# Kernel tuning notes

Hardware: AMD Instinct MI355X
Metric: run time of the kernel (lower is better)

Reference implementation:

```python
import jax, jax.numpy as jnp
import numpy as np

B, S, D, H = 4, 1024, 1024, 16
DK = D // H


def setup_inputs() -> dict:
    key = jax.random.key(0)
    ks = jax.random.split(key, 13)
    s = 1.0 / np.sqrt(D)
    return {
        "query": jax.random.normal(ks[0], (B, S, D), jnp.float32),
        "key": jax.random.normal(ks[1], (B, S, D), jnp.float32),
        "value": jax.random.normal(ks[2], (B, S, D), jnp.float32),
        "mask": jax.random.randint(ks[3], (B, H, S, S), 0, 2).astype(bool),
        "Wq": jax.random.normal(ks[4], (D, D), jnp.float32) * s,
        "bq": jnp.zeros((D,), jnp.float32),
        "Wk": jax.random.normal(ks[5], (D, D), jnp.float32) * s,
        "bk": jnp.zeros((D,), jnp.float32),
        "Wv": jax.random.normal(ks[6], (D, D), jnp.float32) * s,
        "bv": jnp.zeros((D,), jnp.float32),
        "Wo": jax.random.normal(ks[7], (D, D), jnp.float32) * s,
        "bo": jnp.zeros((D,), jnp.float32),
    }


def reference(query, key, value, mask, Wq, bq, Wk, bk, Wv, bv, Wo, bo):
    b = query.shape[0]
    # QKV projections, split heads: [B,S,D] -> [B,H,S,DK]
    q = (query @ Wq + bq).reshape(b, -1, H, DK).transpose(0, 2, 1, 3)
    k = (key @ Wk + bk).reshape(b, -1, H, DK).transpose(0, 2, 1, 3)
    v = (value @ Wv + bv).reshape(b, -1, H, DK).transpose(0, 2, 1, 3)
    # scaled dot-product attention with explicit [B,H,Sq,Sk] scores
    scores = jnp.einsum("bhqd,bhkd->bhqk", q, k) / jnp.sqrt(jnp.float32(DK))
    scores = jnp.where(mask, -jnp.inf, scores)
    attn_weights = jax.nn.softmax(scores, axis=-1)
    attn_out = jnp.einsum("bhqk,bhkd->bhqd", attn_weights, v)
    # merge heads and project out; dropout is identity in eval mode
    attn_out = attn_out.transpose(0, 2, 1, 3).reshape(b, -1, D)
    out = attn_out @ Wo + bo
    return out, attn_weights
```

## Files before the change

### kernel.cpp

```cpp
#include <hip/hip_runtime.h>

typedef __attribute__((ext_vector_type(8))) __bf16   bf16x8;
typedef __attribute__((ext_vector_type(4))) __bf16   bf16x4;
typedef __attribute__((ext_vector_type(8))) _Float16 halfx8;
typedef __attribute__((ext_vector_type(4))) float    floatx4;
typedef __attribute__((ext_vector_type(4))) int      intx4;

#define S_  1024
#define D_  1024
#define H_  16
#define DK_ 64
#define B_  4
#define M_  4096

__device__ __forceinline__ void gload_lds16(const void* g, void* l) {
  __builtin_amdgcn_global_load_lds(
      (const __attribute__((address_space(1))) unsigned int*)g,
      (__attribute__((address_space(3))) unsigned int*)l, 16, 0, 0);
}

__global__ __launch_bounds__(256) void prep(
    const float* __restrict__ q, const float* __restrict__ k,
    const float* __restrict__ v, __bf16* __restrict__ X,
    const float* __restrict__ W0, const float* __restrict__ W1,
    const float* __restrict__ W2, const float* __restrict__ W3,
    __bf16* __restrict__ WT, const unsigned char* __restrict__ m,
    int* __restrict__ flag)
{
  __shared__ __align__(16) unsigned char shb[9216];
  const int bid = blockIdx.x;
  const int t = threadIdx.x;
  if (bid < 6144) {
    const int z = bid >> 11;
    const int bx = bid & 2047;
    const float* src = (z == 0) ? q : (z == 1) ? k : v;
    __bf16* dst = X + (size_t)z * 4194304;
    const size_t idx = ((size_t)bx * 256 + t) * 8;
    floatx4 a = *(const floatx4*)(src + idx);
    floatx4 b = *(const floatx4*)(src + idx + 4);
    bf16x8 o;
#pragma unroll
    for (int j = 0; j < 4; ++j) { o[j] = (__bf16)a[j]; o[4 + j] = (__bf16)b[j]; }
    *(bf16x8*)(dst + idx) = o;
  } else if (bid < 7168) {
    const int g = bid - 6144;
    const int z = g >> 8, yy = (g >> 4) & 15, xx = g & 15;
    const float* W = (z == 0) ? W0 : (z == 1) ? W1 : (z == 2) ? W2 : W3;
    __bf16* O = WT + (size_t)z * (D_ * (size_t)D_);
    __bf16* T = (__bf16*)shb;
    const int r0 = yy * 64, c0 = xx * 64;
#pragma unroll
    for (int it = 0; it < 4; ++it) {
      int idx = t * 4 + it * 1024;
      int r = idx >> 6, c = idx & 63;
      floatx4 a = *(const floatx4*)(W + (size_t)(r0 + r) * D_ + c0 + c);
      bf16x4 o;
#pragma unroll
      for (int j = 0; j < 4; ++j) o[j] = (__bf16)a[j];
      *(bf16x4*)(&T[r * 72 + c]) = o;
    }
    __syncthreads();
#pragma unroll
    for (int it = 0; it < 2; ++it) {
      int idx = t * 8 + it * 2048;
      int orow = idx >> 6, oc = idx & 63;
      bf16x8 vv;
#pragma unroll
      for (int j = 0; j < 8; ++j) vv[j] = T[(oc + j) * 72 + orow];
      *(bf16x8*)(O + (size_t)(c0 + orow) * D_ + (r0 + oc)) = vv;
    }
  } else {
    unsigned* sacc = (unsigned*)shb;
    unsigned acc = 0;
    for (int i = t; i < 4096; i += 256)
      if (i & 3) acc |= m[i];
    sacc[t] = acc;
    __syncthreads();
    if (t == 0) {
      unsigned tot = 0;
      for (int i = 0; i < 256; ++i) tot |= sacc[i];
      flag[0] = tot ? 1 : 0;
    }
  }
}

template <int MODE>
__device__ __forceinline__ void gemm_body(
    const __bf16* __restrict__ X, const __bf16* __restrict__ WT,
    const float* __restrict__ bias, void* __restrict__ outp, __bf16* sh,
    const int m0, const int n0)
{
  __bf16* As = sh;
  __bf16* Bs = sh + 128 * 64;
  const int t = threadIdx.x;
  const int w = t >> 6, lane = t & 63, quad = lane >> 4, cl = lane & 15;
  const int wm = w >> 1, wn = w & 1;
  const int srow = lane >> 3, scol = (lane & 7) * 8;

  floatx4 acc[4][4];
#pragma unroll
  for (int i = 0; i < 4; ++i)
#pragma unroll
    for (int j = 0; j < 4; ++j) acc[i][j] = (floatx4){0.f, 0.f, 0.f, 0.f};

  for (int kt = 0; kt < 16; ++kt) {
    const int k0 = kt * 64;
    __syncthreads();
#pragma unroll
    for (int it = 0; it < 4; ++it) {
      const int ch = it * 4 + w;
      gload_lds16(X  + (size_t)(m0 + ch * 8 + srow) * D_ + k0 + scol, As + ch * 512);
      gload_lds16(WT + (size_t)(n0 + ch * 8 + srow) * D_ + k0 + scol, Bs + ch * 512);
    }
    __syncthreads();
#pragma unroll
    for (int ks = 0; ks < 2; ++ks) {
      bf16x8 a[4], b[4];
#pragma unroll
      for (int mt = 0; mt < 4; ++mt)
        a[mt] = *(const bf16x8*)(&As[(wm * 64 + mt * 16 + cl) * 64 + ks * 32 + quad * 8]);
#pragma unroll
      for (int nt = 0; nt < 4; ++nt)
        b[nt] = *(const bf16x8*)(&Bs[(wn * 64 + nt * 16 + cl) * 64 + ks * 32 + quad * 8]);
#pragma unroll
      for (int mt = 0; mt < 4; ++mt)
#pragma unroll
        for (int nt = 0; nt < 4; ++nt)
          acc[mt][nt] = __builtin_amdgcn_mfma_f32_16x16x32_bf16(a[mt], b[nt], acc[mt][nt], 0, 0, 0);
    }
  }

  if (MODE <= 2) {
#pragma unroll
    for (int mt = 0; mt < 4; ++mt)
#pragma unroll
      for (int nt = 0; nt < 4; ++nt) {
        const int nl = n0 + wn * 64 + nt * 16 + cl;
        const float bv = bias[nl];
#pragma unroll
        for (int r = 0; r < 4; ++r) {
          const int ml = m0 + wm * 64 + mt * 16 + quad * 4 + r;
          float v = acc[mt][nt][r] + bv;
          if (MODE == 0) {
            ((float*)outp)[(size_t)ml * D_ + nl] = v;
          } else {
            if (MODE == 1) v *= 0.125f;
            const int bb = ml >> 10, ss = ml & 1023, hh = nl >> 6, dd = nl & 63;
            ((_Float16*)outp)[(size_t)((bb * H_ + hh) * S_ + ss) * DK_ + dd] = (_Float16)v;
          }
        }
      }
  } else {
    __syncthreads();
    __bf16* T = sh + w * (64 * 72);
    const int hbase = n0 + wn * 64;
#pragma unroll
    for (int mt = 0; mt < 4; ++mt)
#pragma unroll
      for (int nt = 0; nt < 4; ++nt) {
        const int nl = hbase + nt * 16 + cl;
        const float bv = bias[nl];
        const int dk = nt * 16 + cl;
#pragma unroll
        for (int r = 0; r < 4; ++r) {
          const int sl = mt * 16 + quad * 4 + r;
          T[dk * 72 + sl] = (__bf16)(acc[mt][nt][r] + bv);
        }
      }
    __syncthreads();
    const int bb = m0 >> 10;
    const int hh = hbase >> 6;
    __bf16* out = (__bf16*)outp;
#pragma unroll
    for (int i = 0; i < 8; ++i) {
      int idx = lane * 8 + i * 512;
      int dk = idx >> 6, sl = idx & 63;
      bf16x8 v = *(const bf16x8*)(&T[dk * 72 + sl]);
      int sg = (m0 & 1023) + wm * 64 + sl;
      *(bf16x8*)(out + (size_t)((bb * H_ + hh) * DK_ + dk) * S_ + sg) = v;
    }
  }
}

__global__ __launch_bounds__(256) void gemm_qkv(
    const __bf16* __restrict__ Xbf, const __bf16* __restrict__ wt,
    const float* __restrict__ bq, const float* __restrict__ bk,
    const float* __restrict__ bv,
    void* __restrict__ Qo, void* __restrict__ Ko, void* __restrict__ Vto)
{
  __shared__ __bf16 sh[18432];
  const int z = blockIdx.z;
  const int m0 = blockIdx.x * 128, n0 = blockIdx.y * 128;
  if (z == 0)      gemm_body<1>(Xbf,               wt,               bq, Qo,  sh, m0, n0);
  else if (z == 1) gemm_body<2>(Xbf + 4194304,     wt + 1048576,     bk, Ko,  sh, m0, n0);
  else             gemm_body<3>(Xbf + 2 * 4194304, wt + 2 * 1048576, bv, Vto, sh, m0, n0);
}

__global__ __launch_bounds__(256) void gemm_out(
    const __bf16* __restrict__ X, const __bf16* __restrict__ WT,
    const float* __restrict__ bias, float* __restrict__ outp)
{
  __shared__ __bf16 sh[18432];
  gemm_body<0>(X, WT, bias, (void*)outp, sh, blockIdx.x * 128, blockIdx.y * 128);
}

__global__ __launch_bounds__(512, 1) void attn_kernel(
    const _Float16* __restrict__ Q, const _Float16* __restrict__ K,
    const __bf16* __restrict__ Vt, const unsigned char* __restrict__ maskB,
    const int* __restrict__ mflag, float* __restrict__ attnW,
    __bf16* __restrict__ AO)
{
  __shared__ __align__(16) unsigned char smem[150784];
  __bf16*        P   = (__bf16*)smem;
  _Float16*      Qs  = (_Float16*)smem;
  _Float16*      Ks  = (_Float16*)(smem + 131328);
  __bf16*        Vts = (__bf16*)(smem + 140544);
  unsigned char* Ms  = smem + 149760;
  float*         rls = (float*)(smem + 150272);
  float*         S1  = (float*)(smem + 150528);

  const int t = threadIdx.x;
  const int w = t >> 6, lane = t & 63, quad = lane >> 4, cl = lane & 15;
  const int wr = w & 3, wh = w >> 2;
  const int o = blockIdx.x + blockIdx.y * 16;
  const int f = (o & 7) * 128 + (o >> 3);
  const int q0 = (f & 15) * 64;
  const int bh = f >> 4;
  const bool mbyte = (*mflag != 0);
  const int* maskI = (const int*)maskB;
  const long maskbase = (long)bh * S_ * S_;

  {
    const _Float16* g = Q + (size_t)(bh * S_ + q0) * DK_;
    const int idx = t * 8;
    *(halfx8*)(&Qs[(idx >> 6) * 72 + (idx & 63)]) = *(const halfx8*)(g + idx);
  }

  halfx8 kreg;
  bf16x8 vreg;
  intx4  mra, mrb;
  const _Float16* Kbase  = K  + (size_t)bh * S_ * DK_;
  const __bf16*   Vbase  = Vt + (size_t)bh * DK_ * S_;

#define LOAD_TILE(KT)                                                              \
  {                                                                                \
    const int k0_ = (KT) * 64;                                                     \
    kreg = *(const halfx8*)(Kbase + (size_t)k0_ * DK_ + t * 8);                    \
    vreg = *(const bf16x8*)(Vbase + (size_t)(t >> 3) * S_ + k0_ + (t & 7) * 8);    \
    if (mbyte) {                                                                   \
      int2 mv = *(const int2*)(maskB + maskbase +                                  \
                   (size_t)(q0 + (t >> 3)) * S_ + k0_ + (t & 7) * 8);              \
      mra.x = mv.x; mra.y = mv.y;                                                  \
    } else {                                                                       \
      const int* mp = maskI + maskbase + (size_t)(q0 + (t >> 3)) * S_ + k0_ +      \
                      (t & 7) * 8;                                                 \
      mra = *(const intx4*)(mp);                                                   \
      mrb = *(const intx4*)(mp + 4);                                               \
    }                                                                              \
  }

  LOAD_TILE(0);
  __syncthreads();
  const halfx8 a0 = *(const halfx8*)(&Qs[(wr * 16 + cl) * 72 + quad * 8]);
  const halfx8 a1 = *(const halfx8*)(&Qs[(wr * 16 + cl) * 72 + 32 + quad * 8]);

  float lacc[4] = {0.f, 0.f, 0.f, 0.f};
  floatx4 acc_o[4];
#pragma unroll
  for (int i = 0; i < 4; ++i) acc_o[i] = (floatx4){0.f, 0.f, 0.f, 0.f};
  __bf16* Pw = P + (size_t)(wr * 16) * 1026;

  for (int kt = 0; kt < 16; ++kt) {
    const int k0 = kt * 64;
    __syncthreads();

    *(halfx8*)(&Ks[(t >> 3) * 72 + (t & 7) * 8]) = kreg;
    *(bf16x8*)(&Vts[(t >> 3) * 72 + (t & 7) * 8]) = vreg;
    {
      unsigned m8 = 0;
      if (mbyte) {
        unsigned x = (unsigned)mra.x, y = (unsigned)mra.y;
        m8 |= ((x & 0x000000ffu) ? 1u : 0u) << 0;
        m8 |= ((x & 0x0000ff00u) ? 1u : 0u) << 1;
        m8 |= ((x & 0x00ff0000u) ? 1u : 0u) << 2;
        m8 |= ((x & 0xff000000u) ? 1u : 0u) << 3;
        m8 |= ((y & 0x000000ffu) ? 1u : 0u) << 4;
        m8 |= ((y & 0x0000ff00u) ? 1u : 0u) << 5;
        m8 |= ((y & 0x00ff0000u) ? 1u : 0u) << 6;
        m8 |= ((y & 0xff000000u) ? 1u : 0u) << 7;
      } else {
#pragma unroll
        for (int j = 0; j < 4; ++j) {
          m8 |= (mra[j] ? 1u : 0u) << j;
          m8 |= (mrb[j] ? 1u : 0u) << (4 + j);
        }
      }
      Ms[(t >> 3) * 8 + (t & 7)] = (unsigned char)m8;
    }
    __syncthreads();

    unsigned long long mrow[4];
#pragma unroll
    for (int r = 0; r < 4; ++r)
      mrow[r] = ((const unsigned long long*)Ms)[wr * 16 + quad * 4 + r];

    if (kt < 15) LOAD_TILE(kt + 1);

#pragma unroll
    for (int ntl = 0; ntl < 2; ++ntl) {
      const int nt = wh * 2 + ntl;
      floatx4 s = (floatx4){0.f, 0.f, 0.f, 0.f};
      halfx8 b0 = *(const halfx8*)(&Ks[(nt * 16 + cl) * 72 + quad * 8]);
      halfx8 b1 = *(const halfx8*)(&Ks[(nt * 16 + cl) * 72 + 32 + quad * 8]);
      __builtin_amdgcn_s_setprio(1);
      s = __builtin_amdgcn_mfma_f32_16x16x32_f16(a0, b0, s, 0, 0, 0);
      s = __builtin_amdgcn_mfma_f32_16x16x32_f16(a1, b1, s, 0, 0, 0);
      __builtin_amdgcn_s_setprio(0);
#pragma unroll
      for (int r = 0; r < 4; ++r) {
        const int mk = (int)((mrow[r] >> (nt * 16 + cl)) & 1ull);
        float sv = s[r];
        sv = (sv < 25.f) ? sv : 25.f;
        float p = mk ? 0.0f : __expf(sv);
        __bf16 pb = (__bf16)p;
        lacc[r] += (float)pb;
        Pw[(quad * 4 + r) * 1026 + k0 + nt * 16 + cl] = pb;
      }
    }

    __builtin_amdgcn_s_setprio(1);
    {
      bf16x8 a = *(const bf16x8*)(&Pw[cl * 1026 + k0 + wh * 32 + quad * 8]);
#pragma unroll
      for (int nt2 = 0; nt2 < 4; ++nt2) {
        bf16x8 b = *(const bf16x8*)(&Vts[(nt2 * 16 + cl) * 72 + wh * 32 + quad * 8]);
        acc_o[nt2] = __builtin_amdgcn_mfma_f32_16x16x32_bf16(a, b, acc_o[nt2], 0, 0, 0);
      }
    }
    __builtin_amdgcn_s_setprio(0);
  }
#undef LOAD_TILE

  __syncthreads();
  float* Xo = (float*)(smem + 131328);
  if (wh == 1) {
#pragma unroll
    for (int nt2 = 0; nt2 < 4; ++nt2)
#pragma unroll
      for (int j = 0; j < 4; ++j)
        Xo[(wr * 64 + lane) * 16 + nt2 * 4 + j] = acc_o[nt2][j];
#pragma unroll
    for (int r = 0; r < 4; ++r) {
      float v = lacc[r];
      v += __shfl_xor(v, 1); v += __shfl_xor(v, 2);
      v += __shfl_xor(v, 4); v += __shfl_xor(v, 8);
      if (cl == 0) S1[wr * 16 + quad * 4 + r] = v;
    }
  }
  __syncthreads();
  if (wh == 0) {
    const int bb = bh >> 4, hh = bh & 15;
#pragma unroll
    for (int nt2 = 0; nt2 < 4; ++nt2)
#pragma unroll
      for (int j = 0; j < 4; ++j)
        acc_o[nt2][j] += Xo[(wr * 64 + lane) * 16 + nt2 * 4 + j];
#pragma unroll
    for (int r = 0; r < 4; ++r) {
      float v = lacc[r];
      v += __shfl_xor(v, 1); v += __shfl_xor(v, 2);
      v += __shfl_xor(v, 4); v += __shfl_xor(v, 8);
      v += S1[wr * 16 + quad * 4 + r];
      const int rowg = q0 + wr * 16 + quad * 4 + r;
      const float rl = (v > 0.f) ? 1.0f / v : 0.f;
      if (cl == 0) rls[wr * 16 + quad * 4 + r] = rl;
#pragma unroll
      for (int nt2 = 0; nt2 < 4; ++nt2) {
        float o2 = acc_o[nt2][r] * rl;
        AO[(size_t)(bb * S_ + rowg) * D_ + hh * DK_ + nt2 * 16 + cl] = (__bf16)o2;
      }
    }
  }
  __syncthreads();

#pragma unroll
  for (int rr = 0; rr < 8; ++rr) {
    const int row = w * 8 + rr;
    const float rlv = rls[row];
    float* g = attnW + ((size_t)(bh * S_) + q0 + row) * S_;
    const __bf16* prow = &P[(size_t)row * 1026];
#pragma unroll
    for (int i = 0; i < 4; ++i) {
      const int c = lane * 4 + i * 256;
      bf16x4 pv = *(const bf16x4*)(prow + c);
      floatx4 ov;
#pragma unroll
      for (int j = 0; j < 4; ++j) ov[j] = (float)pv[j] * rlv;
      *(floatx4*)(g + c) = ov;
    }
  }
}

extern "C" void kernel_launch(void* const* d_in, const int* in_sizes, int n_in,
                              void* d_out, int out_size, void* d_ws, size_t ws_size,
                              hipStream_t stream)
{
  (void)in_sizes; (void)n_in; (void)out_size; (void)ws_size;
  const float* query = (const float*)d_in[0];
  const float* key   = (const float*)d_in[1];
  const float* value = (const float*)d_in[2];
  const unsigned char* mask = (const unsigned char*)d_in[3];
  const float* Wq = (const float*)d_in[4];
  const float* bq = (const float*)d_in[5];
  const float* Wk = (const float*)d_in[6];
  const float* bk = (const float*)d_in[7];
  const float* Wv = (const float*)d_in[8];
  const float* bv = (const float*)d_in[9];
  const float* Wo = (const float*)d_in[10];
  const float* bo = (const float*)d_in[11];

  __bf16* ws = (__bf16*)d_ws;
  __bf16*   wt   = ws;
  _Float16* Qws  = (_Float16*)(ws + 4  * 1048576);
  _Float16* Kws  = (_Float16*)(ws + 8  * 1048576);
  __bf16*   Vtws = ws + 12 * 1048576;
  __bf16*   AOws = ws + 16 * 1048576;
  __bf16*   Xbf  = ws + 20 * 1048576;
  int*      mfl  = (int*)(ws + 32 * 1048576 + 131072);

  float* outO  = (float*)d_out;
  float* attnW = outO + 4 * 1048576;

  prep<<<7169, 256, 0, stream>>>(query, key, value, Xbf, Wq, Wk, Wv, Wo, wt, mask, mfl);
  gemm_qkv<<<dim3(32, 8, 3), 256, 0, stream>>>(Xbf, wt, bq, bk, bv,
                                               (void*)Qws, (void*)Kws, (void*)Vtws);
  attn_kernel<<<dim3(16, 64), 512, 0, stream>>>(Qws, Kws, Vtws, mask, mfl,
                                                attnW, AOws);
  gemm_out<<<dim3(32, 8), 256, 0, stream>>>(AOws, wt + 3 * 1048576, bo, outO);
}
```

Before: 620.7 us.

## Pre-pack attention mask into bitmasks in prep and double-buffer K/V tile loads

Moves the conversion of the mask into 64-bit row bitmasks out of the attention kernel and into extra blocks of the prep kernel, writing a packed mask buffer to the workspace. The dtype probe becomes its own single-block launch ahead of prep. The attention kernel then reads only one 64-bit word per row per tile instead of raw mask bytes, and uses two register buffers so loads run two tiles ahead. This trades an extra launch and packing pass, which still reads the full mask, for less mask traffic and bit-packing work inside the attention loop.

```diff
diff --git a/kernel.cpp b/kernel.cpp
--- a/kernel.cpp
+++ b/kernel.cpp
@@ -19,13 +19,30 @@
       (__attribute__((address_space(3))) unsigned int*)l, 16, 0, 0);
 }
 
+__global__ __launch_bounds__(256) void mask_probe(const unsigned char* __restrict__ m,
+                                                  int* __restrict__ flag)
+{
+  __shared__ unsigned sacc[256];
+  const int t = threadIdx.x;
+  unsigned acc = 0;
+  for (int i = t; i < 4096; i += 256)
+    if (i & 3) acc |= m[i];
+  sacc[t] = acc;
+  __syncthreads();
+  if (t == 0) {
+    unsigned tot = 0;
+    for (int i = 0; i < 256; ++i) tot |= sacc[i];
+    flag[0] = tot ? 1 : 0;
+  }
+}
+
 __global__ __launch_bounds__(256) void prep(
     const float* __restrict__ q, const float* __restrict__ k,
     const float* __restrict__ v, __bf16* __restrict__ X,
     const float* __restrict__ W0, const float* __restrict__ W1,
     const float* __restrict__ W2, const float* __restrict__ W3,
     __bf16* __restrict__ WT, const unsigned char* __restrict__ m,
-    int* __restrict__ flag)
+    const int* __restrict__ flag, unsigned long long* __restrict__ PM)
 {
   __shared__ __align__(16) unsigned char shb[9216];
   const int bid = blockIdx.x;
@@ -70,17 +87,37 @@
       *(bf16x8*)(O + (size_t)(c0 + orow) * D_ + (r0 + oc)) = vv;
     }
   } else {
-    unsigned* sacc = (unsigned*)shb;
-    unsigned acc = 0;
-    for (int i = t; i < 4096; i += 256)
-      if (i & 3) acc |= m[i];
-    sacc[t] = acc;
-    __syncthreads();
-    if (t == 0) {
-      unsigned tot = 0;
-      for (int i = 0; i < 256; ++i) tot |= sacc[i];
-      flag[0] = tot ? 1 : 0;
-    }
+    const int pid = (bid - 7168) * 256 + t;
+    const int s   = pid & 1023;
+    const int ktq = (pid >> 10) & 15;
+    const int bhp = pid >> 14;
+    unsigned long long bits = 0;
+    if (*flag) {
+      const unsigned char* mp = m + (size_t)bhp * 1048576 + (size_t)s * 1024 + ktq * 64;
+#pragma unroll
+      for (int i = 0; i < 4; ++i) {
+        intx4 vv = *(const intx4*)(mp + i * 16);
+#pragma unroll
+        for (int j = 0; j < 4; ++j) {
+          unsigned x = (unsigned)vv[j];
+          const int bb = i * 16 + j * 4;
+          bits |= (unsigned long long)((x & 0x000000ffu) ? 1u : 0u) << (bb + 0);
+          bits |= (unsigned long long)((x & 0x0000ff00u) ? 1u : 0u) << (bb + 1);
+          bits |= (unsigned long long)((x & 0x00ff0000u) ? 1u : 0u) << (bb + 2);
+          bits |= (unsigned long long)((x & 0xff000000u) ? 1u : 0u) << (bb + 3);
+        }
+      }
+    } else {
+      const int* mi = (const int*)m + (size_t)bhp * 1048576 + (size_t)s * 1024 + ktq * 64;
+#pragma unroll
+      for (int i = 0; i < 16; ++i) {
+        intx4 vv = *(const intx4*)(mi + i * 4);
+#pragma unroll
+        for (int j = 0; j < 4; ++j)
+          bits |= (unsigned long long)(vv[j] ? 1u : 0u) << (i * 4 + j);
+      }
+    }
+    PM[pid] = bits;
   }
 }
 
@@ -206,16 +243,15 @@
 
 __global__ __launch_bounds__(512, 1) void attn_kernel(
     const _Float16* __restrict__ Q, const _Float16* __restrict__ K,
-    const __bf16* __restrict__ Vt, const unsigned char* __restrict__ maskB,
-    const int* __restrict__ mflag, float* __restrict__ attnW,
-    __bf16* __restrict__ AO)
+    const __bf16* __restrict__ Vt, const unsigned long long* __restrict__ PM,
+    float* __restrict__ attnW, __bf16* __restrict__ AO)
 {
   __shared__ __align__(16) unsigned char smem[150784];
   __bf16*        P   = (__bf16*)smem;
   _Float16*      Qs  = (_Float16*)smem;
   _Float16*      Ks  = (_Float16*)(smem + 131328);
   __bf16*        Vts = (__bf16*)(smem + 140544);
-  unsigned char* Ms  = smem + 149760;
+  unsigned long long* Ms = (unsigned long long*)(smem + 149760);
   float*         rls = (float*)(smem + 150272);
   float*         S1  = (float*)(smem + 150528);
 
@@ -226,9 +262,6 @@
   const int f = (o & 7) * 128 + (o >> 3);
   const int q0 = (f & 15) * 64;
   const int bh = f >> 4;
-  const bool mbyte = (*mflag != 0);
-  const int* maskI = (const int*)maskB;
-  const long maskbase = (long)bh * S_ * S_;
 
   {
     const _Float16* g = Q + (size_t)(bh * S_ + q0) * DK_;
@@ -236,30 +269,70 @@
     *(halfx8*)(&Qs[(idx >> 6) * 72 + (idx & 63)]) = *(const halfx8*)(g + idx);
   }
 
-  halfx8 kreg;
-  bf16x8 vreg;
-  intx4  mra, mrb;
   const _Float16* Kbase  = K  + (size_t)bh * S_ * DK_;
   const __bf16*   Vbase  = Vt + (size_t)bh * DK_ * S_;
-
-#define LOAD_TILE(KT)                                                              \
+  const unsigned long long* PMbase = PM + ((size_t)bh * 16) * 1024 + q0;
+
+  halfx8 kA, kB;
+  bf16x8 vA, vB;
+  unsigned long long mA = 0, mB = 0;
+
+#define LOAD_TILE(KR, VR, MR, KT)                                                  \
   {                                                                                \
     const int k0_ = (KT) * 64;                                                     \
-    kreg = *(const halfx8*)(Kbase + (size_t)k0_ * DK_ + t * 8);                    \
-    vreg = *(const bf16x8*)(Vbase + (size_t)(t >> 3) * S_ + k0_ + (t & 7) * 8);    \
-    if (mbyte) {                                                                   \
-      int2 mv = *(const int2*)(maskB + maskbase +                                  \
-                   (size_t)(q0 + (t >> 3)) * S_ + k0_ + (t & 7) * 8);              \
-      mra.x = mv.x; mra.y = mv.y;                                                  \
-    } else {                                                                       \
-      const int* mp = maskI + maskbase + (size_t)(q0 + (t >> 3)) * S_ + k0_ +      \
-                      (t & 7) * 8;                                                 \
-      mra = *(const intx4*)(mp);                                                   \
-      mrb = *(const intx4*)(mp + 4);                                               \
+    KR = *(const halfx8*)(Kbase + (size_t)k0_ * DK_ + t * 8);                      \
+    VR = *(const bf16x8*)(Vbase + (size_t)(t >> 3) * S_ + k0_ + (t & 7) * 8);      \
+    if (t < 64) MR = PMbase[(size_t)(KT) * 1024 + t];                              \
+  }
+
+#define STAGE_TILE(KR, VR, MR)                                                     \
+  {                                                                                \
+    *(halfx8*)(&Ks[(t >> 3) * 72 + (t & 7) * 8]) = KR;                             \
+    *(bf16x8*)(&Vts[(t >> 3) * 72 + (t & 7) * 8]) = VR;                            \
+    if (t < 64) Ms[t] = MR;                                                        \
+  }
+
+#define COMPUTE_TILE(KT)                                                           \
+  {                                                                                \
+    const int k0 = (KT) * 64;                                                      \
+    unsigned long long mrow[4];                                                    \
+    _Pragma("unroll")                                                              \
+    for (int r = 0; r < 4; ++r) mrow[r] = Ms[wr * 16 + quad * 4 + r];              \
+    _Pragma("unroll")                                                              \
+    for (int ntl = 0; ntl < 2; ++ntl) {                                            \
+      const int nt = wh * 2 + ntl;                                                 \
+      floatx4 s = (floatx4){0.f, 0.f, 0.f, 0.f};                                   \
+      halfx8 b0 = *(const halfx8*)(&Ks[(nt * 16 + cl) * 72 + quad * 8]);           \
+      halfx8 b1 = *(const halfx8*)(&Ks[(nt * 16 + cl) * 72 + 32 + quad * 8]);      \
+      __builtin_amdgcn_s_setprio(1);                                               \
+      s = __builtin_amdgcn_mfma_f32_16x16x32_f16(a0, b0, s, 0, 0, 0);              \
+      s = __builtin_amdgcn_mfma_f32_16x16x32_f16(a1, b1, s, 0, 0, 0);              \
+      __builtin_amdgcn_s_setprio(0);                                               \
+      _Pragma("unroll")                                                            \
+      for (int r = 0; r < 4; ++r) {                                                \
+        const int mk = (int)((mrow[r] >> (nt * 16 + cl)) & 1ull);                  \
+        float sv = s[r];                                                           \
+        sv = (sv < 25.f) ? sv : 25.f;                                              \
+        float p = mk ? 0.0f : __expf(sv);                                          \
+        __bf16 pb = (__bf16)p;                                                     \
+        lacc[r] += (float)pb;                                                      \
+        Pw[(quad * 4 + r) * 1026 + k0 + nt * 16 + cl] = pb;                        \
+      }                                                                            \
     }                                                                              \
-  }
-
-  LOAD_TILE(0);
+    __builtin_amdgcn_s_setprio(1);                                                 \
+    {                                                                              \
+      bf16x8 a = *(const bf16x8*)(&Pw[cl * 1026 + k0 + wh * 32 + quad * 8]);       \
+      _Pragma("unroll")                                                            \
+      for (int nt2 = 0; nt2 < 4; ++nt2) {                                          \
+        bf16x8 b = *(const bf16x8*)(&Vts[(nt2 * 16 + cl) * 72 + wh * 32 + quad * 8]); \
+        acc_o[nt2] = __builtin_amdgcn_mfma_f32_16x16x32_bf16(a, b, acc_o[nt2], 0, 0, 0); \
+      }                                                                            \
+    }                                                                              \
+    __builtin_amdgcn_s_setprio(0);                                                 \
+  }
+
+  LOAD_TILE(kA, vA, mA, 0);
+  LOAD_TILE(kB, vB, mB, 1);
   __syncthreads();
   const halfx8 a0 = *(const halfx8*)(&Qs[(wr * 16 + cl) * 72 + quad * 8]);
   const halfx8 a1 = *(const halfx8*)(&Qs[(wr * 16 + cl) * 72 + 32 + quad * 8]);
@@ -270,76 +343,22 @@
   for (int i = 0; i < 4; ++i) acc_o[i] = (floatx4){0.f, 0.f, 0.f, 0.f};
   __bf16* Pw = P + (size_t)(wr * 16) * 1026;
 
-  for (int kt = 0; kt < 16; ++kt) {
-    const int k0 = kt * 64;
-    __syncthreads();
-
-    *(halfx8*)(&Ks[(t >> 3) * 72 + (t & 7) * 8]) = kreg;
-    *(bf16x8*)(&Vts[(t >> 3) * 72 + (t & 7) * 8]) = vreg;
-    {
-      unsigned m8 = 0;
-      if (mbyte) {
-        unsigned x = (unsigned)mra.x, y = (unsigned)mra.y;
-        m8 |= ((x & 0x000000ffu) ? 1u : 0u) << 0;
-        m8 |= ((x & 0x0000ff00u) ? 1u : 0u) << 1;
-        m8 |= ((x & 0x00ff0000u) ? 1u : 0u) << 2;
-        m8 |= ((x & 0xff000000u) ? 1u : 0u) << 3;
-        m8 |= ((y & 0x000000ffu) ? 1u : 0u) << 4;
-        m8 |= ((y & 0x0000ff00u) ? 1u : 0u) << 5;
-        m8 |= ((y & 0x00ff0000u) ? 1u : 0u) << 6;
-        m8 |= ((y & 0xff000000u) ? 1u : 0u) << 7;
-      } else {
-#pragma unroll
-        for (int j = 0; j < 4; ++j) {
-          m8 |= (mra[j] ? 1u : 0u) << j;
-          m8 |= (mrb[j] ? 1u : 0u) << (4 + j);
-        }
-      }
-      Ms[(t >> 3) * 8 + (t & 7)] = (unsigned char)m8;
-    }
-    __syncthreads();
-
-    unsigned long long mrow[4];
-#pragma unroll
-    for (int r = 0; r < 4; ++r)
-      mrow[r] = ((const unsigned long long*)Ms)[wr * 16 + quad * 4 + r];
-
-    if (kt < 15) LOAD_TILE(kt + 1);
-
-#pragma unroll
-    for (int ntl = 0; ntl < 2; ++ntl) {
-      const int nt = wh * 2 + ntl;
-      floatx4 s = (floatx4){0.f, 0.f, 0.f, 0.f};
-      halfx8 b0 = *(const halfx8*)(&Ks[(nt * 16 + cl) * 72 + quad * 8]);
-      halfx8 b1 = *(const halfx8*)(&Ks[(nt * 16 + cl) * 72 + 32 + quad * 8]);
-      __builtin_amdgcn_s_setprio(1);
-      s = __builtin_amdgcn_mfma_f32_16x16x32_f16(a0, b0, s, 0, 0, 0);
-      s = __builtin_amdgcn_mfma_f32_16x16x32_f16(a1, b1, s, 0, 0, 0);
-      __builtin_amdgcn_s_setprio(0);
-#pragma unroll
-      for (int r = 0; r < 4; ++r) {
-        const int mk = (int)((mrow[r] >> (nt * 16 + cl)) & 1ull);
-        float sv = s[r];
-        sv = (sv < 25.f) ? sv : 25.f;
-        float p = mk ? 0.0f : __expf(sv);
-        __bf16 pb = (__bf16)p;
-        lacc[r] += (float)pb;
-        Pw[(quad * 4 + r) * 1026 + k0 + nt * 16 + cl] = pb;
-      }
-    }
-
-    __builtin_amdgcn_s_setprio(1);
-    {
-      bf16x8 a = *(const bf16x8*)(&Pw[cl * 1026 + k0 + wh * 32 + quad * 8]);
-#pragma unroll
-      for (int nt2 = 0; nt2 < 4; ++nt2) {
-        bf16x8 b = *(const bf16x8*)(&Vts[(nt2 * 16 + cl) * 72 + wh * 32 + quad * 8]);
-        acc_o[nt2] = __builtin_amdgcn_mfma_f32_16x16x32_bf16(a, b, acc_o[nt2], 0, 0, 0);
-      }
-    }
-    __builtin_amdgcn_s_setprio(0);
+  for (int kt2 = 0; kt2 < 8; ++kt2) {
+    const int kt = kt2 * 2;
+    __syncthreads();
+    STAGE_TILE(kA, vA, mA);
+    __syncthreads();
+    if (kt2 < 7) LOAD_TILE(kA, vA, mA, kt + 2);
+    COMPUTE_TILE(kt);
+    __syncthreads();
+    STAGE_TILE(kB, vB, mB);
+    __syncthreads();
+    if (kt2 < 7) LOAD_TILE(kB, vB, mB, kt + 3);
+    COMPUTE_TILE(kt + 1);
   }
 #undef LOAD_TILE
+#undef STAGE_TILE
+#undef COMPUTE_TILE
 
   __syncthreads();
   float* Xo = (float*)(smem + 131328);
@@ -427,14 +446,16 @@
   __bf16*   AOws = ws + 16 * 1048576;
   __bf16*   Xbf  = ws + 20 * 1048576;
   int*      mfl  = (int*)(ws + 32 * 1048576 + 131072);
+  unsigned long long* PM = (unsigned long long*)(ws + 34 * 1048576);
 
   float* outO  = (float*)d_out;
   float* attnW = outO + 4 * 1048576;
 
-  prep<<<7169, 256, 0, stream>>>(query, key, value, Xbf, Wq, Wk, Wv, Wo, wt, mask, mfl);
+  mask_probe<<<1, 256, 0, stream>>>(mask, mfl);
+  prep<<<11264, 256, 0, stream>>>(query, key, value, Xbf, Wq, Wk, Wv, Wo, wt,
+                                  mask, mfl, PM);
   gemm_qkv<<<dim3(32, 8, 3), 256, 0, stream>>>(Xbf, wt, bq, bk, bv,
                                                (void*)Qws, (void*)Kws, (void*)Vtws);
-  attn_kernel<<<dim3(16, 64), 512, 0, stream>>>(Qws, Kws, Vtws, mask, mfl,
-                                                attnW, AOws);
+  attn_kernel<<<dim3(16, 64), 512, 0, stream>>>(Qws, Kws, Vtws, PM, attnW, AOws);
   gemm_out<<<dim3(32, 8), 256, 0, stream>>>(AOws, wt + 3 * 1048576, bo, outO);
 }
```

Result: slower. 697.1 us (+12.3%).
